# Optimization experiments

Hardware: AMD Instinct MI355X
Metric: run time of the kernel (lower is better)

Reference implementation:

```python
import jax, jax.numpy as jnp
import numpy as np

N = 50000      # nodes
E = 400000     # edges (before self-loops)
D_IN = 128     # input node features
H1, C1 = 8, 64   # layer-1 heads / per-head channels (concat -> 512)
H2, C2 = 1, 16   # layer-2 heads / per-head channels (mean -> 16)
NEG_SLOPE = 0.2  # PyG GATConv default leaky-relu slope


def setup_inputs() -> dict:
    key = jax.random.key(0)
    ks = jax.random.split(key, 10)
    x = jax.random.normal(ks[0], (N, D_IN), jnp.float32)
    edge_index = jax.random.randint(ks[1], (2, E), 0, N, dtype=jnp.int32)
    s1 = D_IN ** -0.5
    s2 = (H1 * C1) ** -0.5
    return {
        "x": x,
        "edge_index": edge_index,
        "W1": jax.random.normal(ks[2], (D_IN, H1 * C1), jnp.float32) * s1,
        "a1_src": jax.random.normal(ks[3], (H1, C1), jnp.float32) * (C1 ** -0.5),
        "a1_dst": jax.random.normal(ks[4], (H1, C1), jnp.float32) * (C1 ** -0.5),
        "b1": jnp.zeros((H1 * C1,), jnp.float32),
        "W2": jax.random.normal(ks[5], (H1 * C1, H2 * C2), jnp.float32) * s2,
        "a2_src": jax.random.normal(ks[6], (H2, C2), jnp.float32) * (C2 ** -0.5),
        "a2_dst": jax.random.normal(ks[7], (H2, C2), jnp.float32) * (C2 ** -0.5),
        "b2": jnp.zeros((C2,), jnp.float32),
    }


def gat_layer(x, W, a_src, a_dst, bias, src, dst, H, C, concat):
    n = x.shape[0]
    h = (x @ W).reshape(n, H, C)                       # [N,H,C]
    # per-node attention halves (PyG: alpha = a_src . h_src + a_dst . h_dst)
    al_src = jnp.einsum('nhc,hc->nh', h, a_src)        # [N,H]
    al_dst = jnp.einsum('nhc,hc->nh', h, a_dst)
    logits = jax.nn.leaky_relu(al_src[src] + al_dst[dst], NEG_SLOPE)  # [E,H]
    # segment softmax over incoming edges of each destination node
    m = jax.ops.segment_max(logits, dst, num_segments=n)
    e = jnp.exp(logits - m[dst])
    denom = jax.ops.segment_sum(e, dst, num_segments=n)
    alpha = e / denom[dst]                             # [E,H]
    out = jax.ops.segment_sum(alpha[:, :, None] * h[src], dst, num_segments=n)  # [N,H,C]
    out = out.reshape(n, H * C) if concat else out.mean(axis=1)
    return out + bias


def reference(x, edge_index, W1, a1_src, a1_dst, b1, W2, a2_src, a2_dst, b2):
    n = x.shape[0]
    # PyG GATConv adds self-loops by default (applied in each layer)
    loops = jnp.arange(n, dtype=edge_index.dtype)
    src = jnp.concatenate([edge_index[0], loops])
    dst = jnp.concatenate([edge_index[1], loops])
    h1 = gat_layer(x, W1, a1_src, a1_dst, b1, src, dst, H1, C1, True)   # [N,512]
    h1 = jax.nn.elu(h1)
    return gat_layer(h1, W2, a2_src, a2_dst, b2, src, dst, H2, C2, False)  # [N,16]
```

## Files before the change

### kernel.cpp

```cpp
#include <hip/hip_runtime.h>
#include <math.h>

#define N_NODES 50000
#define N_EDGES 400000
#define N_TOT   450000
#define NEG 0.2f
#define CAP 64

typedef __attribute__((ext_vector_type(8))) short bf16x8;
typedef __attribute__((ext_vector_type(8))) unsigned short u16x8;
typedef __attribute__((ext_vector_type(4))) float f32x4;

__device__ __forceinline__ float lrelu(float x) { return x > 0.f ? x : NEG * x; }

__device__ __forceinline__ unsigned short f2bf(float f) {
    unsigned u = __float_as_uint(f);
    unsigned r = u + 0x7FFFu + ((u >> 16) & 1u);
    return (unsigned short)(r >> 16);
}
__device__ __forceinline__ float bf2f(unsigned short h) {
    return __uint_as_float(((unsigned)h) << 16);
}

__global__ void k_init(const float* __restrict__ W1, unsigned short* W1hiT,
                       const float* __restrict__ W2, unsigned short* W2hiT,
                       const float* __restrict__ a1s, const float* __restrict__ a1d,
                       unsigned short* W1aThi, unsigned short* W1aTlo,
                       int* cursor) {
    int i = blockIdx.x * 256 + threadIdx.x;
    if (i < 128 * 512) {
        int col = i & 511, k = i >> 9;
        W1hiT[col * 128 + k] = f2bf(W1[k * 512 + col]);
    } else if (i < 128 * 512 + 512 * 16) {
        int j = i - 128 * 512;
        int col = j & 15, k = j >> 4;
        W2hiT[col * 512 + k] = f2bf(W2[k * 16 + col]);
    } else if (i < 128 * 512 + 512 * 16 + 128 * 16) {
        int j = i - (128 * 512 + 512 * 16);
        int c16 = j & 15, k = j >> 4;
        int hd = c16 & 7;
        const float* av = (c16 < 8) ? a1s : a1d;
        float acc = 0.f;
#pragma unroll 8
        for (int c = 0; c < 64; c++)
            acc = fmaf(W1[k * 512 + hd * 64 + c], av[hd * 64 + c], acc);
        unsigned short h = f2bf(acc);
        W1aThi[c16 * 128 + k] = h;
        W1aTlo[c16 * 128 + k] = f2bf(acc - bf2f(h));
    } else {
        int j = i - (128 * 512 + 512 * 16 + 128 * 16);
        if (j < N_NODES) cursor[j] = 0;
    }
}

#define SCAT 256
__global__ __launch_bounds__(256) void k_sg1(const int* __restrict__ ei,
                                             int* __restrict__ cursor,
                                             int* __restrict__ colsrc,
                                             const float* __restrict__ x,
                                             const unsigned short* __restrict__ W1hiT,
                                             const unsigned short* __restrict__ W1aThi,
                                             const unsigned short* __restrict__ W1aTlo,
                                             unsigned short* __restrict__ h1b,
                                             float* __restrict__ al1s,
                                             float* __restrict__ al1d) {
    __shared__ unsigned short xs_hi[64 * 136];
    if (blockIdx.x < SCAT) {
        int gtid = blockIdx.x * 256 + threadIdx.x;
        for (int i = gtid; i < N_TOT; i += SCAT * 256) {
            int src, dst;
            if (i < N_EDGES) { src = ei[i]; dst = ei[N_EDGES + i]; }
            else             { src = dst = i - N_EDGES; }
            int pos = atomicAdd(&cursor[dst], 1);
            if (pos < CAP) colsrc[dst * CAP + pos] = src;
        }
        return;
    }
    const int t = threadIdx.x;
    const int rb = (blockIdx.x - SCAT) * 64;

#pragma unroll
    for (int i = 0; i < 8; i++) {
        int idx = t + 256 * i;
        int r = idx >> 5;
        int k = (idx & 31) * 4;
        int gr = rb + r;
        float4 v = make_float4(0.f, 0.f, 0.f, 0.f);
        if (gr < N_NODES) v = *reinterpret_cast<const float4*>(&x[gr * 128 + k]);
        ushort4 hi;
        hi.x = f2bf(v.x); hi.y = f2bf(v.y); hi.z = f2bf(v.z); hi.w = f2bf(v.w);
        *reinterpret_cast<ushort4*>(&xs_hi[r * 136 + k]) = hi;
    }
    __syncthreads();

    const int lane = t & 63;
    const int w = t >> 6;
    const int kbase = (lane >> 4) * 8;
    const int colloc = (w << 4) + (lane & 15);

#pragma unroll
    for (int pr = 0; pr < 4; pr++) {
        bf16x8 bhi[2][4];
#pragma unroll
        for (int si = 0; si < 2; si++) {
            int col = (pr * 2 + si) * 64 + colloc;
#pragma unroll
            for (int kc = 0; kc < 4; kc++)
                bhi[si][kc] = *reinterpret_cast<const bf16x8*>(&W1hiT[col * 128 + kc * 32 + kbase]);
        }
#pragma unroll
        for (int mt = 0; mt < 4; mt++) {
            const int arow = mt * 16 + (lane & 15);
            bf16x8 ah[4];
#pragma unroll
            for (int kc = 0; kc < 4; kc++)
                ah[kc] = *reinterpret_cast<const bf16x8*>(&xs_hi[arow * 136 + kc * 32 + kbase]);
#pragma unroll
            for (int si = 0; si < 2; si++) {
                f32x4 acc = {0.f, 0.f, 0.f, 0.f};
#pragma unroll
                for (int kc = 0; kc < 4; kc++)
                    acc = __builtin_amdgcn_mfma_f32_16x16x32_bf16(ah[kc], bhi[si][kc], acc, 0, 0, 0);
                const int col = (pr * 2 + si) * 64 + colloc;
                const int r0 = rb + mt * 16 + (lane >> 4) * 4;
#pragma unroll
                for (int r = 0; r < 4; r++) {
                    int row = r0 + r;
                    if (row < N_NODES) h1b[row * 512 + col] = f2bf(acc[r]);
                }
            }
        }
    }

    {
        const int c16 = lane & 15;
        bf16x8 bh[4], bl[4];
#pragma unroll
        for (int kc = 0; kc < 4; kc++) {
            bh[kc] = *reinterpret_cast<const bf16x8*>(&W1aThi[c16 * 128 + kc * 32 + kbase]);
            bl[kc] = *reinterpret_cast<const bf16x8*>(&W1aTlo[c16 * 128 + kc * 32 + kbase]);
        }
        const int arow = (w << 4) + (lane & 15);
        f32x4 acc = {0.f, 0.f, 0.f, 0.f};
#pragma unroll
        for (int kc = 0; kc < 4; kc++) {
            bf16x8 ah = *reinterpret_cast<const bf16x8*>(&xs_hi[arow * 136 + kc * 32 + kbase]);
            acc = __builtin_amdgcn_mfma_f32_16x16x32_bf16(ah, bh[kc], acc, 0, 0, 0);
            acc = __builtin_amdgcn_mfma_f32_16x16x32_bf16(ah, bl[kc], acc, 0, 0, 0);
        }
        const int r0 = rb + (w << 4) + (lane >> 4) * 4;
#pragma unroll
        for (int r = 0; r < 4; r++) {
            int row = r0 + r;
            if (row < N_NODES) {
                if (c16 < 8) al1s[row * 8 + c16] = acc[r];
                else         al1d[row * 8 + (c16 - 8)] = acc[r];
            }
        }
    }
}

__global__ __launch_bounds__(256) void k_agg1(const int* __restrict__ cursor,
                                              const int* __restrict__ colsrc,
                                              const float* __restrict__ al1s,
                                              const float* __restrict__ al1d,
                                              const unsigned short* __restrict__ h1b,
                                              const float* __restrict__ b1,
                                              const unsigned short* __restrict__ W2hiT,
                                              const float* __restrict__ a2s,
                                              const float* __restrict__ a2d,
                                              unsigned short* __restrict__ h2b,
                                              float* __restrict__ al2s,
                                              float* __restrict__ al2d) {
    __shared__ float pw[4][8 * 66];
    __shared__ __align__(16) unsigned short vs[4 * 520];
    const int wid  = threadIdx.x >> 6;
    const int lane = threadIdx.x & 63;
    const int n0 = blockIdx.x * 4;
    const int n  = n0 + wid;
    const int cnt = min(cursor[n], CAP);
    const int eb = n * CAP;
    const int h  = lane >> 3;
    const int c8 = lane << 3;
    float* mypw = pw[wid];

    const float4 d0 = *reinterpret_cast<const float4*>(&al1d[n * 8]);
    const float4 d1 = *reinterpret_cast<const float4*>(&al1d[n * 8 + 4]);

    int s0 = 0;
    float p[8];
    if (lane < cnt) {
        s0 = colsrc[eb + lane];
        const float4 u0 = *reinterpret_cast<const float4*>(&al1s[s0 * 8]);
        const float4 u1 = *reinterpret_cast<const float4*>(&al1s[s0 * 8 + 4]);
        p[0] = __expf(fminf(lrelu(u0.x + d0.x), 60.f));
        p[1] = __expf(fminf(lrelu(u0.y + d0.y), 60.f));
        p[2] = __expf(fminf(lrelu(u0.z + d0.z), 60.f));
        p[3] = __expf(fminf(lrelu(u0.w + d0.w), 60.f));
        p[4] = __expf(fminf(lrelu(u1.x + d1.x), 60.f));
        p[5] = __expf(fminf(lrelu(u1.y + d1.y), 60.f));
        p[6] = __expf(fminf(lrelu(u1.z + d1.z), 60.f));
        p[7] = __expf(fminf(lrelu(u1.w + d1.w), 60.f));
    } else {
#pragma unroll
        for (int hh = 0; hh < 8; hh++) p[hh] = 0.f;
        s0 = 0;
    }
#pragma unroll
    for (int hh = 0; hh < 8; hh++) mypw[hh * 66 + lane] = p[hh];

    float acc[8] = {0.f, 0.f, 0.f, 0.f, 0.f, 0.f, 0.f, 0.f};
    float sm = 0.f;
    const int pwh = h * 66;
    const int cnt4 = (cnt + 3) & ~3;
    const int G = cnt4 >> 2;

    u16x8 vA[4], vB[4];

    auto LD = [&](u16x8* dst, int jj) {
#pragma unroll
        for (int k = 0; k < 4; k++) {
            int s = __shfl(s0, jj + k, 64);
            dst[k] = *reinterpret_cast<const u16x8*>(&h1b[s * 512 + c8]);
        }
    };
    auto CONS = [&](const u16x8* src, int jj) {
#pragma unroll
        for (int k = 0; k < 4; k++) {
            float w = mypw[pwh + jj + k];
            sm += w;
#pragma unroll
            for (int c = 0; c < 8; c++)
                acc[c] = fmaf(w, bf2f(src[k][c]), acc[c]);
        }
    };

    LD(vA, 0);
    if (G > 1) LD(vB, 4);
    int g = 0;
    for (; g + 2 < G; g += 2) {
        CONS(vA, g * 4);       LD(vA, (g + 2) * 4);
        CONS(vB, g * 4 + 4);   if (g + 3 < G) LD(vB, (g + 3) * 4);
    }
    if (g < G)     CONS(vA, g * 4);
    if (g + 1 < G) CONS(vB, g * 4 + 4);

    const float inv = 1.f / sm;
    const float4 ba = *reinterpret_cast<const float4*>(&b1[c8]);
    const float4 bb = *reinterpret_cast<const float4*>(&b1[c8 + 4]);
    float v[8];
    v[0] = acc[0] * inv + ba.x; v[1] = acc[1] * inv + ba.y;
    v[2] = acc[2] * inv + ba.z; v[3] = acc[3] * inv + ba.w;
    v[4] = acc[4] * inv + bb.x; v[5] = acc[5] * inv + bb.y;
    v[6] = acc[6] * inv + bb.z; v[7] = acc[7] * inv + bb.w;
#pragma unroll
    for (int k = 0; k < 8; k++)
        v[k] = v[k] > 0.f ? v[k] : __expf(v[k]) - 1.f;
    u16x8 o;
#pragma unroll
    for (int k = 0; k < 8; k++) o[k] = f2bf(v[k]);
    *reinterpret_cast<u16x8*>(&vs[wid * 520 + c8]) = o;

    __syncthreads();

    if (wid == 0) {
        const int col   = lane & 15;
        const int kbase = (lane >> 4) << 3;
        const int rowm  = lane & 3;
        f32x4 a2 = {0.f, 0.f, 0.f, 0.f};
#pragma unroll 4
        for (int kc = 0; kc < 16; kc++) {
            bf16x8 bh = *reinterpret_cast<const bf16x8*>(&W2hiT[col * 512 + kc * 32 + kbase]);
            bf16x8 ah = *reinterpret_cast<const bf16x8*>(&vs[rowm * 520 + kc * 32 + kbase]);
            a2 = __builtin_amdgcn_mfma_f32_16x16x32_bf16(ah, bh, a2, 0, 0, 0);
        }
        if (lane < 16) {
            const float as_c = a2s[col];
            const float ad_c = a2d[col];
#pragma unroll
            for (int r = 0; r < 4; r++) {
                float ps = a2[r] * as_c;
                float pd = a2[r] * ad_c;
                ps += __shfl_xor(ps, 1, 64); pd += __shfl_xor(pd, 1, 64);
                ps += __shfl_xor(ps, 2, 64); pd += __shfl_xor(pd, 2, 64);
                ps += __shfl_xor(ps, 4, 64); pd += __shfl_xor(pd, 4, 64);
                ps += __shfl_xor(ps, 8, 64); pd += __shfl_xor(pd, 8, 64);
                h2b[(n0 + r) * 16 + col] = f2bf(a2[r]);
                if (lane == 0) { al2s[n0 + r] = ps; al2d[n0 + r] = pd; }
            }
        }
    }
}

__global__ __launch_bounds__(256) void k_agg2(const int* __restrict__ cursor,
                                              const int* __restrict__ colsrc,
                                              const float* __restrict__ al2s,
                                              const float* __restrict__ al2d,
                                              const unsigned short* __restrict__ h2b,
                                              const float* __restrict__ b2,
                                              float* __restrict__ out) {
    int wv = threadIdx.x >> 6, lane = threadIdx.x & 63;
    int n = blockIdx.x * 4 + wv;
    if (n >= N_NODES) return;
    int cnt = min(cursor[n], CAP);
    const int eb = n * CAP;
    float ald = al2d[n];
    int q = lane >> 3;
    int c2 = (lane & 7) << 1;
    float acc0 = 0.f, acc1 = 0.f, smL = 0.f;
    for (int e = q; e < cnt; e += 8) {
        int s = colsrc[eb + e];
        float w = __expf(fminf(lrelu(al2s[s] + ald), 60.f));
        unsigned v = *reinterpret_cast<const unsigned*>(&h2b[s * 16 + c2]);
        smL += w;
        acc0 = fmaf(w, bf2f((unsigned short)(v & 0xFFFFu)), acc0);
        acc1 = fmaf(w, __uint_as_float(v & 0xFFFF0000u), acc1);
    }
    acc0 += __shfl_xor(acc0, 8, 64);  acc1 += __shfl_xor(acc1, 8, 64);  smL += __shfl_xor(smL, 8, 64);
    acc0 += __shfl_xor(acc0, 16, 64); acc1 += __shfl_xor(acc1, 16, 64); smL += __shfl_xor(smL, 16, 64);
    acc0 += __shfl_xor(acc0, 32, 64); acc1 += __shfl_xor(acc1, 32, 64); smL += __shfl_xor(smL, 32, 64);
    if (q == 0) {
        float inv = 1.f / smL;
        float2 r;
        r.x = acc0 * inv + b2[c2];
        r.y = acc1 * inv + b2[c2 + 1];
        *reinterpret_cast<float2*>(&out[n * 16 + c2]) = r;
    }
}

extern "C" void kernel_launch(void* const* d_in, const int* in_sizes, int n_in,
                              void* d_out, int out_size, void* d_ws, size_t ws_size,
                              hipStream_t stream) {
    const float* x   = (const float*)d_in[0];
    const int*   ei  = (const int*)d_in[1];
    const float* W1  = (const float*)d_in[2];
    const float* a1s = (const float*)d_in[3];
    const float* a1d = (const float*)d_in[4];
    const float* b1  = (const float*)d_in[5];
    const float* W2  = (const float*)d_in[6];
    const float* a2s = (const float*)d_in[7];
    const float* a2d = (const float*)d_in[8];
    const float* b2  = (const float*)d_in[9];
    float* out = (float*)d_out;

    char* ws = (char*)d_ws;
    unsigned short* h1b = (unsigned short*)(ws + 0);
    unsigned short* h2b = (unsigned short*)(ws + 102400000);
    float* al1s = (float*)(ws + 105600000);
    float* al1d = (float*)(ws + 107200000);
    float* al2s = (float*)(ws + 108800000);
    float* al2d = (float*)(ws + 109000000);
    int* cursor = (int*)(ws + 109200000);
    int* colsrc = (int*)(ws + 109400000);
    unsigned short* W1hiT  = (unsigned short*)(ws + 122200000);
    unsigned short* W2hiT  = (unsigned short*)(ws + 122336000);
    unsigned short* W1aThi = (unsigned short*)(ws + 122352384);
    unsigned short* W1aTlo = (unsigned short*)(ws + 122356480);

    k_init<<<492, 256, 0, stream>>>(W1, W1hiT, W2, W2hiT, a1s, a1d, W1aThi, W1aTlo, cursor);

    k_sg1<<<SCAT + (N_NODES + 63) / 64, 256, 0, stream>>>(ei, cursor, colsrc, x,
                                                          W1hiT, W1aThi, W1aTlo,
                                                          h1b, al1s, al1d);

    k_agg1<<<(N_NODES + 3) / 4, 256, 0, stream>>>(cursor, colsrc, al1s, al1d, h1b, b1,
                                                  W2hiT, a2s, a2d, h2b, al2s, al2d);

    k_agg2<<<(N_NODES + 3) / 4, 256, 0, stream>>>(cursor, colsrc, al2s, al2d, h2b, b2, out);
}
```

Before: 223.1 us.

## Compute layer-2 projection per wave and simplify gather loop in agg1

Each wave now runs its own MFMA for the layer-2 projection of its node, which removes the block-wide __syncthreads and leaves no waves idle while wave 0 handles all four nodes. Only row 0 of each MFMA tile is used, so the MFMA work grows fourfold. The double-buffered software-pipelined gather loop becomes a plain unroll-by-4 loop with a scalar tail. That cuts register pressure but leaves overlapping loads with compute to the compiler.

```diff
diff --git a/kernel.cpp b/kernel.cpp
--- a/kernel.cpp
+++ b/kernel.cpp
@@ -173,11 +173,10 @@
                                               float* __restrict__ al2s,
                                               float* __restrict__ al2d) {
     __shared__ float pw[4][8 * 66];
-    __shared__ __align__(16) unsigned short vs[4 * 520];
+    __shared__ __align__(16) unsigned short vsw[4][528];
     const int wid  = threadIdx.x >> 6;
     const int lane = threadIdx.x & 63;
-    const int n0 = blockIdx.x * 4;
-    const int n  = n0 + wid;
+    const int n = blockIdx.x * 4 + wid;
     const int cnt = min(cursor[n], CAP);
     const int eb = n * CAP;
     const int h  = lane >> 3;
@@ -204,7 +203,6 @@
     } else {
 #pragma unroll
         for (int hh = 0; hh < 8; hh++) p[hh] = 0.f;
-        s0 = 0;
     }
 #pragma unroll
     for (int hh = 0; hh < 8; hh++) mypw[hh * 66 + lane] = p[hh];
@@ -212,38 +210,34 @@
     float acc[8] = {0.f, 0.f, 0.f, 0.f, 0.f, 0.f, 0.f, 0.f};
     float sm = 0.f;
     const int pwh = h * 66;
-    const int cnt4 = (cnt + 3) & ~3;
-    const int G = cnt4 >> 2;
-
-    u16x8 vA[4], vB[4];
-
-    auto LD = [&](u16x8* dst, int jj) {
+
+    int j = 0;
+    for (; j + 3 < cnt; j += 4) {
+        int s[4]; float w[4]; u16x8 vv[4];
 #pragma unroll
         for (int k = 0; k < 4; k++) {
-            int s = __shfl(s0, jj + k, 64);
-            dst[k] = *reinterpret_cast<const u16x8*>(&h1b[s * 512 + c8]);
-        }
-    };
-    auto CONS = [&](const u16x8* src, int jj) {
+            s[k] = __shfl(s0, j + k, 64);
+            w[k] = mypw[pwh + j + k];
+        }
+#pragma unroll
+        for (int k = 0; k < 4; k++)
+            vv[k] = *reinterpret_cast<const u16x8*>(&h1b[s[k] * 512 + c8]);
 #pragma unroll
         for (int k = 0; k < 4; k++) {
-            float w = mypw[pwh + jj + k];
-            sm += w;
+            sm += w[k];
 #pragma unroll
             for (int c = 0; c < 8; c++)
-                acc[c] = fmaf(w, bf2f(src[k][c]), acc[c]);
-        }
-    };
-
-    LD(vA, 0);
-    if (G > 1) LD(vB, 4);
-    int g = 0;
-    for (; g + 2 < G; g += 2) {
-        CONS(vA, g * 4);       LD(vA, (g + 2) * 4);
-        CONS(vB, g * 4 + 4);   if (g + 3 < G) LD(vB, (g + 3) * 4);
-    }
-    if (g < G)     CONS(vA, g * 4);
-    if (g + 1 < G) CONS(vB, g * 4 + 4);
+                acc[c] = fmaf(w[k], bf2f(vv[k][c]), acc[c]);
+        }
+    }
+    for (; j < cnt; ++j) {
+        int s = __shfl(s0, j, 64);
+        u16x8 v = *reinterpret_cast<const u16x8*>(&h1b[s * 512 + c8]);
+        float w = mypw[pwh + j];
+        sm += w;
+#pragma unroll
+        for (int c = 0; c < 8; c++) acc[c] = fmaf(w, bf2f(v[c]), acc[c]);
+    }
 
     const float inv = 1.f / sm;
     const float4 ba = *reinterpret_cast<const float4*>(&b1[c8]);
@@ -259,36 +253,27 @@
     u16x8 o;
 #pragma unroll
     for (int k = 0; k < 8; k++) o[k] = f2bf(v[k]);
-    *reinterpret_cast<u16x8*>(&vs[wid * 520 + c8]) = o;
-
-    __syncthreads();
-
-    if (wid == 0) {
+    *reinterpret_cast<u16x8*>(&vsw[wid][c8]) = o;
+
+    {
         const int col   = lane & 15;
         const int kbase = (lane >> 4) << 3;
-        const int rowm  = lane & 3;
         f32x4 a2 = {0.f, 0.f, 0.f, 0.f};
 #pragma unroll 4
         for (int kc = 0; kc < 16; kc++) {
             bf16x8 bh = *reinterpret_cast<const bf16x8*>(&W2hiT[col * 512 + kc * 32 + kbase]);
-            bf16x8 ah = *reinterpret_cast<const bf16x8*>(&vs[rowm * 520 + kc * 32 + kbase]);
+            bf16x8 ah = *reinterpret_cast<const bf16x8*>(&vsw[wid][kc * 32 + kbase]);
             a2 = __builtin_amdgcn_mfma_f32_16x16x32_bf16(ah, bh, a2, 0, 0, 0);
         }
-        if (lane < 16) {
-            const float as_c = a2s[col];
-            const float ad_c = a2d[col];
-#pragma unroll
-            for (int r = 0; r < 4; r++) {
-                float ps = a2[r] * as_c;
-                float pd = a2[r] * ad_c;
-                ps += __shfl_xor(ps, 1, 64); pd += __shfl_xor(pd, 1, 64);
-                ps += __shfl_xor(ps, 2, 64); pd += __shfl_xor(pd, 2, 64);
-                ps += __shfl_xor(ps, 4, 64); pd += __shfl_xor(pd, 4, 64);
-                ps += __shfl_xor(ps, 8, 64); pd += __shfl_xor(pd, 8, 64);
-                h2b[(n0 + r) * 16 + col] = f2bf(a2[r]);
-                if (lane == 0) { al2s[n0 + r] = ps; al2d[n0 + r] = pd; }
-            }
-        }
+        const float ov = a2[0];
+        float ps = ov * a2s[col];
+        float pd = ov * a2d[col];
+        ps += __shfl_xor(ps, 1, 64); pd += __shfl_xor(pd, 1, 64);
+        ps += __shfl_xor(ps, 2, 64); pd += __shfl_xor(pd, 2, 64);
+        ps += __shfl_xor(ps, 4, 64); pd += __shfl_xor(pd, 4, 64);
+        ps += __shfl_xor(ps, 8, 64); pd += __shfl_xor(pd, 8, 64);
+        if (lane < 16) h2b[n * 16 + col] = f2bf(ov);
+        if (lane == 0) { al2s[n] = ps; al2d[n] = pd; }
     }
 }
 
```

New measurement: 265.7 us. 1.19x slower.
